# Kernel tuning notes

Measured on AMD Instinct MI355X. Metric: run time of the kernel, lower is better.

The kernel has to match this reference:

```python
import jax, jax.numpy as jnp
import numpy as np

N = 40000   # nodes
E = 640000  # edges (before self-loops)
G = 64      # graphs
EPS = 1e-5


def _gat_conv(x, src, dst, W, a_src, a_dst, bias, n_nodes):
    """PyG GATConv, heads=1, leaky_relu slope 0.2, with self-loops already in src/dst."""
    h = x @ W.T                              # [N, out]
    s_score = h @ a_src                      # [N]
    d_score = h @ a_dst                      # [N]
    e = jax.nn.leaky_relu(s_score[src] + d_score[dst], 0.2)  # [E]
    m = jax.ops.segment_max(e, dst, num_segments=n_nodes)
    ex = jnp.exp(e - m[dst])
    z = jax.ops.segment_sum(ex, dst, num_segments=n_nodes)
    alpha = ex / z[dst]                      # per-dst softmax over incoming edges
    out = jax.ops.segment_sum(h[src] * alpha[:, None], dst, num_segments=n_nodes)
    return out + bias


def _layer_norm(x, gamma, beta):
    mu = jnp.mean(x, axis=-1, keepdims=True)
    var = jnp.mean((x - mu) ** 2, axis=-1, keepdims=True)
    return gamma * (x - mu) * jax.lax.rsqrt(var + EPS) + beta


def setup_inputs() -> dict:
    key = jax.random.key(0)
    ks = jax.random.split(key, 16)
    x = jax.random.normal(ks[0], (N, 128), dtype=jnp.float32)
    edge_index = jax.random.randint(ks[1], (2, E), 0, N, dtype=jnp.int32)
    batch = jnp.sort(jax.random.randint(ks[2], (N,), 0, G, dtype=jnp.int32))
    def glorot(k, shape):
        fan = shape[-1]
        return jax.random.normal(k, shape, dtype=jnp.float32) / jnp.sqrt(jnp.float32(fan))
    return {
        "x": x, "edge_index": edge_index, "batch": batch,
        "W1": glorot(ks[3], (128, 128)), "a1_src": glorot(ks[4], (128,)),
        "a1_dst": glorot(ks[5], (128,)), "b1": jnp.zeros((128,), jnp.float32),
        "g1": jnp.ones((128,), jnp.float32), "be1": jnp.zeros((128,), jnp.float32),
        "W2": glorot(ks[6], (64, 128)), "a2_src": glorot(ks[7], (64,)),
        "a2_dst": glorot(ks[8], (64,)), "b2": jnp.zeros((64,), jnp.float32),
        "g2": jnp.ones((64,), jnp.float32), "be2": jnp.zeros((64,), jnp.float32),
        "Wl": glorot(ks[9], (64, 64)), "bl": jnp.zeros((64,), jnp.float32),
        "Wc": glorot(ks[10], (1, 64)), "bc": jnp.zeros((1,), jnp.float32),
    }


def reference(x, edge_index, batch, W1, a1_src, a1_dst, b1, g1, be1,
              W2, a2_src, a2_dst, b2, g2, be2, Wl, bl, Wc, bc):
    # add self-loops as PyG GATConv does by default
    loops = jnp.arange(N, dtype=edge_index.dtype)
    src = jnp.concatenate([edge_index[0], loops])
    dst = jnp.concatenate([edge_index[1], loops])

    h = jax.nn.relu(_gat_conv(x, src, dst, W1, a1_src, a1_dst, b1, N))
    h = _layer_norm(h, g1, be1)
    h = jax.nn.relu(_gat_conv(h, src, dst, W2, a2_src, a2_dst, b2, N))
    h = _layer_norm(h, g2, be2)

    # global mean pool over graphs
    sums = jax.ops.segment_sum(h, batch, num_segments=G)          # [G, 64]
    cnt = jax.ops.segment_sum(jnp.ones((N,), h.dtype), batch, num_segments=G)
    pooled = sums / jnp.maximum(cnt, 1.0)[:, None]

    out = pooled @ Wl.T + bl
    out = out @ Wc.T + bc                                          # [G, 1]
    return out.squeeze(-1)                                         # [G]
```

## Files before the change

kernel.cpp:

```cpp
#include <hip/hip_runtime.h>
#include <hip/hip_fp16.h>
#include <math.h>

#define NNODES 40000
#define NEDGES 640000
#define NGRAPH 64
#define CAP 96
constexpr float LN_EPS = 1e-5f;


typedef _Float16 v8h __attribute__((ext_vector_type(8)));
typedef float    v4f __attribute__((ext_vector_type(4)));

__device__ __forceinline__ float bf_sum(float v) {
    #pragma unroll
    for (int o = 32; o > 0; o >>= 1) v += __shfl_xor(v, o);
    return v;
}

__global__ void prep(const float* __restrict__ W1, const float* __restrict__ W2,
                     _Float16* __restrict__ Bf1, _Float16* __restrict__ Bf2,
                     int* __restrict__ cnt, float* __restrict__ sums) {
    int t = blockIdx.x * 256 + threadIdx.x;
    if (t < NNODES) cnt[t] = 0;
    if (t < 128 * 128) {
        const int o = t >> 7, k = t & 127;
        const int nt = o >> 4, lc = o & 15;
        const int ks = k >> 5, g = (k >> 3) & 3, j = k & 7;
        Bf1[(size_t)(((nt * 4 + ks) * 64 + g * 16 + lc) * 8 + j)] = (_Float16)W1[t];
    }
    if (t < 64 * 128) {
        const int o = t >> 7, k = t & 127;
        const int nt = o >> 4, lc = o & 15;
        const int ks = k >> 5, g = (k >> 3) & 3, j = k & 7;
        Bf2[(size_t)(((nt * 4 + ks) * 64 + g * 16 + lc) * 8 + j)] = (_Float16)W2[t];
    }
    if (t < NGRAPH * 64) sums[t] = 0.f;
}

__global__ void bin_edges(const int* __restrict__ ei, int E,
                          int* __restrict__ cnt, unsigned short* __restrict__ ssrc) {
    int e = blockIdx.x * blockDim.x + threadIdx.x;
    if (e >= E) return;
    int s = ei[e], d = ei[E + e];
    int pos = atomicAdd(cnt + d, 1);
    if (pos < CAP) ssrc[d * CAP + pos] = (unsigned short)s;
}

template<int DOUT>
__global__ __launch_bounds__(256) void gemm_scores_mfma(
        const float* __restrict__ X, const _Float16* __restrict__ Bfrag,
        const float* __restrict__ asrc, const float* __restrict__ adst,
        __half* __restrict__ H, float* __restrict__ S, float* __restrict__ Dv) {
    constexpr int NT = DOUT / 16;
    const int lane = threadIdx.x & 63;
    const int wv   = threadIdx.x >> 6;
    const int nb   = blockIdx.x * 64 + wv * 16;
    const int lc = lane & 15, g = lane >> 4;

    v8h a[4];
    const float* xr = X + (size_t)(nb + lc) * 128 + g * 8;
    #pragma unroll
    for (int ks = 0; ks < 4; ++ks) {
        const float4 lo = *(const float4*)(xr + ks * 32);
        const float4 hi = *(const float4*)(xr + ks * 32 + 4);
        v8h av;
        av[0] = (_Float16)lo.x; av[1] = (_Float16)lo.y;
        av[2] = (_Float16)lo.z; av[3] = (_Float16)lo.w;
        av[4] = (_Float16)hi.x; av[5] = (_Float16)hi.y;
        av[6] = (_Float16)hi.z; av[7] = (_Float16)hi.w;
        a[ks] = av;
    }

    v4f acc[NT];
    #pragma unroll
    for (int nt = 0; nt < NT; ++nt) acc[nt] = (v4f){0.f, 0.f, 0.f, 0.f};

    #pragma unroll
    for (int ks = 0; ks < 4; ++ks) {
        #pragma unroll
        for (int nt = 0; nt < NT; ++nt) {
            const v8h bv = *(const v8h*)(Bfrag + (size_t)(((nt * 4 + ks) * 64 + lane) * 8));
            acc[nt] = __builtin_amdgcn_mfma_f32_16x16x32_f16(a[ks], bv, acc[nt], 0, 0, 0);
        }
    }

    float sp[4] = {0.f, 0.f, 0.f, 0.f}, dp[4] = {0.f, 0.f, 0.f, 0.f};
    #pragma unroll
    for (int nt = 0; nt < NT; ++nt) {
        const float as_ = asrc[nt * 16 + lc];
        const float ad_ = adst[nt * 16 + lc];
        #pragma unroll
        for (int r = 0; r < 4; ++r) {
            const float hv = acc[nt][r];
            H[(size_t)(nb + g * 4 + r) * DOUT + nt * 16 + lc] = __float2half_rn(hv);
            sp[r] += hv * as_;
            dp[r] += hv * ad_;
        }
    }
    #pragma unroll
    for (int o = 8; o > 0; o >>= 1) {
        #pragma unroll
        for (int r = 0; r < 4; ++r) {
            sp[r] += __shfl_xor(sp[r], o);
            dp[r] += __shfl_xor(dp[r], o);
        }
    }
    #pragma unroll
    for (int r = 0; r < 4; ++r) {
        if (lc == r) {
            S[nb + g * 4 + r]  = sp[r];
            Dv[nb + g * 4 + r] = dp[r];
        }
    }
}

template<int D>
__device__ __forceinline__ void aggr_one_generic(
        const int node, const int deg, const int lane,
        const unsigned short* __restrict__ ssrc, const float* __restrict__ S,
        const float dsc, const __half* __restrict__ H,
        float& acc0, float& acc1, float& z) {
    constexpr int VPL = D / 64;
    float zz = 0.f;
    const int r0 = node * CAP;
    for (int bse = 0; bse < deg; bse += 64) {
        const int n = min(64, deg - bse);
        int s = 0; float a = 0.f;
        if (lane < n) {
            s = ssrc[r0 + bse + lane];
            float t = S[s] + dsc;
            t = t > 0.f ? t : 0.2f * t;
            a = __expf(t);
        }
        zz += bf_sum(a);
        const int abits = __float_as_int(a);
        for (int j = 0; j < n; ++j) {
            const int sj = __builtin_amdgcn_readlane(s, j);
            const float aj = __int_as_float(__builtin_amdgcn_readlane(abits, j));
            const __half* hp = H + (size_t)sj * D;
            if (VPL == 1) {
                acc0 += aj * __half2float(hp[lane]);
            } else {
                const float2 f = __half22float2(*(const __half2*)(hp + 2 * lane));
                acc0 += aj * f.x; acc1 += aj * f.y;
            }
        }
    }
    z = zz;
}

template<int D, int POOL>
__device__ __forceinline__ void finish_node(
        const int node, const int lane,
        float acc0, float acc1, float z, const float aself, const float2 selfF,
        const float* __restrict__ b, const float* __restrict__ gam,
        const float* __restrict__ bet,
        float* __restrict__ out, const int* __restrict__ batch,
        float* __restrict__ sums) {
    constexpr int VPL = D / 64;
    acc0 += aself * selfF.x;
    if (VPL == 2) acc1 += aself * selfF.y;
    z += aself;
    const float zinv = 1.0f / z;
    float vv[VPL], lsum = 0.f;
    vv[0] = acc0;
    if (VPL == 2) vv[1] = acc1;
    #pragma unroll
    for (int k = 0; k < VPL; ++k) {
        const int ch = VPL * lane + k;
        vv[k] = fmaxf(vv[k] * zinv + b[ch], 0.f);
        lsum += vv[k];
    }
    const float mu = bf_sum(lsum) / D;
    float q = 0.f;
    #pragma unroll
    for (int k = 0; k < VPL; ++k) { vv[k] -= mu; q += vv[k] * vv[k]; }
    const float rstd = rsqrtf(bf_sum(q) / D + LN_EPS);
    #pragma unroll
    for (int k = 0; k < VPL; ++k) {
        const int ch = VPL * lane + k;
        vv[k] = gam[ch] * vv[k] * rstd + bet[ch];
    }
    if (POOL) {
        const int bg = batch[node];
        atomicAdd(&sums[bg * D + lane], vv[0]);
    } else {
        if (VPL == 1) out[(size_t)node * D + lane] = vv[0];
        else *(float2*)(out + (size_t)node * D + 2 * lane) = make_float2(vv[0], vv[1]);
    }
}

template<int D, int POOL>
__global__ __launch_bounds__(256) void gat_aggr(
        const int* __restrict__ cnt, const unsigned short* __restrict__ ssrc,
        const float* __restrict__ S, const float* __restrict__ Dv,
        const __half* __restrict__ H,
        const float* __restrict__ b, const float* __restrict__ gam,
        const float* __restrict__ bet,
        float* __restrict__ out, const int* __restrict__ batch,
        float* __restrict__ sums) {
    constexpr int VPL = D / 64;
    const int lane = threadIdx.x & 63;
    const int wv   = threadIdx.x >> 6;
    const int nodeA = blockIdx.x * 8 + wv * 2;
    const int nodeB = nodeA + 1;

    const int degA = min(__builtin_amdgcn_readfirstlane(cnt[nodeA]), CAP);
    const int degB = min(__builtin_amdgcn_readfirstlane(cnt[nodeB]), CAP);
    const float dscA = Dv[nodeA], dscB = Dv[nodeB];

    float tsA = S[nodeA] + dscA; tsA = tsA > 0.f ? tsA : 0.2f * tsA;
    float tsB = S[nodeB] + dscB; tsB = tsB > 0.f ? tsB : 0.2f * tsB;
    const float aselfA = __expf(tsA);
    const float aselfB = __expf(tsB);

    float2 selfFA, selfFB;
    if (VPL == 1) {
        selfFA = make_float2(__half2float(H[(size_t)nodeA * D + lane]), 0.f);
        selfFB = make_float2(__half2float(H[(size_t)nodeB * D + lane]), 0.f);
    } else {
        selfFA = __half22float2(*(const __half2*)(H + (size_t)nodeA * D + 2 * lane));
        selfFB = __half22float2(*(const __half2*)(H + (size_t)nodeB * D + 2 * lane));
    }

    float accA0 = 0.f, accA1 = 0.f, accB0 = 0.f, accB1 = 0.f;
    float zA, zB;

    if (degA <= 64 && degB <= 64) {
        int sA = 0, sB = 0;
        if (lane < degA) sA = ssrc[nodeA * CAP + lane];
        if (lane < degB) sB = ssrc[nodeB * CAP + lane];
        float tA = S[sA] + dscA;
        float tB = S[sB] + dscB;
        tA = tA > 0.f ? tA : 0.2f * tA;
        tB = tB > 0.f ? tB : 0.2f * tB;
        const float aA = (lane < degA) ? __expf(tA) : 0.f;
        const float aB = (lane < degB) ? __expf(tB) : 0.f;
        zA = bf_sum(aA);
        zB = bf_sum(aB);
        const int abA = __float_as_int(aA), abB = __float_as_int(aB);

        const int nmA = (degA + 7) & ~7;
        const int nmB = (degB + 7) & ~7;
        const int nmax = max(nmA, nmB);
        for (int j = 0; j < nmax; j += 8) {
            const bool doA = j < nmA, doB = j < nmB;
            float afA[8], afB[8];
            __half2 hvA[8], hvB[8];
            __half hsA[8], hsB[8];
            if (doA) {
                #pragma unroll
                for (int u = 0; u < 8; ++u) {
                    const int sj = __builtin_amdgcn_readlane(sA, j + u);
                    afA[u] = __int_as_float(__builtin_amdgcn_readlane(abA, j + u));
                    const __half* hp = H + (size_t)sj * D;
                    if (VPL == 1) hsA[u] = hp[lane];
                    else          hvA[u] = *(const __half2*)(hp + 2 * lane);
                }
            }
            if (doB) {
                #pragma unroll
                for (int u = 0; u < 8; ++u) {
                    const int sj = __builtin_amdgcn_readlane(sB, j + u);
                    afB[u] = __int_as_float(__builtin_amdgcn_readlane(abB, j + u));
                    const __half* hp = H + (size_t)sj * D;
                    if (VPL == 1) hsB[u] = hp[lane];
                    else          hvB[u] = *(const __half2*)(hp + 2 * lane);
                }
            }
            if (doA) {
                #pragma unroll
                for (int u = 0; u < 8; ++u) {
                    if (VPL == 1) {
                        accA0 += afA[u] * __half2float(hsA[u]);
                    } else {
                        accA0 += afA[u] * __half2float(__low2half(hvA[u]));
                        accA1 += afA[u] * __half2float(__high2half(hvA[u]));
                    }
                }
            }
            if (doB) {
                #pragma unroll
                for (int u = 0; u < 8; ++u) {
                    if (VPL == 1) {
                        accB0 += afB[u] * __half2float(hsB[u]);
                    } else {
                        accB0 += afB[u] * __half2float(__low2half(hvB[u]));
                        accB1 += afB[u] * __half2float(__high2half(hvB[u]));
                    }
                }
            }
        }
    } else {
        aggr_one_generic<D>(nodeA, degA, lane, ssrc, S, dscA, H, accA0, accA1, zA);
        aggr_one_generic<D>(nodeB, degB, lane, ssrc, S, dscB, H, accB0, accB1, zB);
    }

    finish_node<D, POOL>(nodeA, lane, accA0, accA1, zA, aselfA, selfFA,
                         b, gam, bet, out, batch, sums);
    finish_node<D, POOL>(nodeB, lane, accB0, accB1, zB, aselfB, selfFB,
                         b, gam, bet, out, batch, sums);
}

__global__ void final_head(const float* __restrict__ sums, const int* __restrict__ batch,
                           const float* __restrict__ Wl, const float* __restrict__ bl,
                           const float* __restrict__ Wc, const float* __restrict__ bc,
                           float* __restrict__ out) {
    __shared__ float p[64];
    __shared__ float red[64];
    const int g = blockIdx.x, tid = threadIdx.x;
    int lo = 0, hi = NNODES;
    while (lo < hi) { int mid = (lo + hi) >> 1; if (batch[mid] < g) lo = mid + 1; else hi = mid; }
    int lo2 = lo, hi2 = NNODES;
    while (lo2 < hi2) { int mid = (lo2 + hi2) >> 1; if (batch[mid] < g + 1) lo2 = mid + 1; else hi2 = mid; }
    const float cnt = (float)(lo2 - lo);
    p[tid] = sums[g * 64 + tid] / fmaxf(cnt, 1.0f);
    __syncthreads();
    float t = bl[tid];
    #pragma unroll 8
    for (int k = 0; k < 64; ++k) t += Wl[tid * 64 + k] * p[k];
    red[tid] = Wc[tid] * t;
    __syncthreads();
    for (int s = 32; s > 0; s >>= 1) {
        if (tid < s) red[tid] += red[tid + s];
        __syncthreads();
    }
    if (tid == 0) out[g] = red[0] + bc[0];
}

extern "C" void kernel_launch(void* const* d_in, const int* in_sizes, int n_in,
                              void* d_out, int out_size, void* d_ws, size_t ws_size,
                              hipStream_t stream) {
    const int N = NNODES, E = NEDGES, G = NGRAPH;

    const float* x      = (const float*)d_in[0];
    const int*   ei     = (const int*)d_in[1];
    const int*   batch  = (const int*)d_in[2];
    const float* W1     = (const float*)d_in[3];
    const float* a1s    = (const float*)d_in[4];
    const float* a1d    = (const float*)d_in[5];
    const float* b1     = (const float*)d_in[6];
    const float* g1     = (const float*)d_in[7];
    const float* be1    = (const float*)d_in[8];
    const float* W2     = (const float*)d_in[9];
    const float* a2s    = (const float*)d_in[10];
    const float* a2d    = (const float*)d_in[11];
    const float* b2     = (const float*)d_in[12];
    const float* g2     = (const float*)d_in[13];
    const float* be2    = (const float*)d_in[14];
    const float* Wl     = (const float*)d_in[15];
    const float* bl     = (const float*)d_in[16];
    const float* Wc     = (const float*)d_in[17];
    const float* bc     = (const float*)d_in[18];

    char* w = (char*)d_ws;
    __half* h1  = (__half*)w; w += (size_t)N * 128 * 2;
    float* acc1 = (float*)w; w += (size_t)N * 128 * 4;
    float* S    = (float*)w; w += (size_t)N * 4;
    float* Dv   = (float*)w; w += (size_t)N * 4;
    int* cnt    = (int*)w;   w += (size_t)N * 4;
    unsigned short* ssrc = (unsigned short*)w; w += (size_t)N * CAP * 2;
    _Float16* Bf1 = (_Float16*)w; w += (size_t)128 * 128 * 2;
    _Float16* Bf2 = (_Float16*)w; w += (size_t)64 * 128 * 2;
    float* sums = (float*)w; w += (size_t)G * 64 * 4;
    __half* h2 = h1;

    const int TB = 256;
    const int gridN = (N + 255) / 256;

    prep<<<gridN, 256, 0, stream>>>(W1, W2, Bf1, Bf2, cnt, sums);

    bin_edges<<<(E + TB - 1) / TB, TB, 0, stream>>>(ei, E, cnt, ssrc);

    gemm_scores_mfma<128><<<N / 64, 256, 0, stream>>>(x, Bf1, a1s, a1d, h1, S, Dv);
    gat_aggr<128, 0><<<N / 8, 256, 0, stream>>>(cnt, ssrc, S, Dv, h1, b1, g1, be1,
                                                acc1, nullptr, nullptr);

    gemm_scores_mfma<64><<<N / 64, 256, 0, stream>>>(acc1, Bf2, a2s, a2d, h2, S, Dv);
    gat_aggr<64, 1><<<N / 8, 256, 0, stream>>>(cnt, ssrc, S, Dv, h2, b2, g2, be2,
                                               nullptr, batch, sums);

    final_head<<<G, 64, 0, stream>>>(sums, batch, Wl, bl, Wc, bc, (float*)d_out);
}
```

Baseline: 245.6 us.

## Fuse layer-2 projection and scores into layer-1 aggregation; merge prep with binning

Layer-1 aggregation now applies bias, ReLU and LayerNorm, then does the 128->64 W2 projection and the attention scores in-kernel from an fp16 W2 copy in LDS. This removes the fp32 acc1 round trip and the second MFMA GEMM launch. Prep and edge binning become one kernel plus a memset, and the gather loop handles two nodes per wave with 8-way unrolled loads. In exchange, every block reconverts W2 into LDS and runs a scalar 64x64 dot loop per node, which adds LDS traffic and work per block.

```diff
diff --git a/kernel.cpp b/kernel.cpp
--- a/kernel.cpp
+++ b/kernel.cpp
@@ -18,33 +18,23 @@
     return v;
 }
 
-__global__ void prep(const float* __restrict__ W1, const float* __restrict__ W2,
-                     _Float16* __restrict__ Bf1, _Float16* __restrict__ Bf2,
-                     int* __restrict__ cnt, float* __restrict__ sums) {
-    int t = blockIdx.x * 256 + threadIdx.x;
-    if (t < NNODES) cnt[t] = 0;
+__global__ void bin_prep(const int* __restrict__ ei, int E,
+                         int* __restrict__ cnt, unsigned short* __restrict__ ssrc,
+                         const float* __restrict__ W1, _Float16* __restrict__ Bf1,
+                         float* __restrict__ sums) {
+    const int t = blockIdx.x * blockDim.x + threadIdx.x;
     if (t < 128 * 128) {
         const int o = t >> 7, k = t & 127;
         const int nt = o >> 4, lc = o & 15;
         const int ks = k >> 5, g = (k >> 3) & 3, j = k & 7;
         Bf1[(size_t)(((nt * 4 + ks) * 64 + g * 16 + lc) * 8 + j)] = (_Float16)W1[t];
     }
-    if (t < 64 * 128) {
-        const int o = t >> 7, k = t & 127;
-        const int nt = o >> 4, lc = o & 15;
-        const int ks = k >> 5, g = (k >> 3) & 3, j = k & 7;
-        Bf2[(size_t)(((nt * 4 + ks) * 64 + g * 16 + lc) * 8 + j)] = (_Float16)W2[t];
-    }
     if (t < NGRAPH * 64) sums[t] = 0.f;
-}
-
-__global__ void bin_edges(const int* __restrict__ ei, int E,
-                          int* __restrict__ cnt, unsigned short* __restrict__ ssrc) {
-    int e = blockIdx.x * blockDim.x + threadIdx.x;
-    if (e >= E) return;
-    int s = ei[e], d = ei[E + e];
-    int pos = atomicAdd(cnt + d, 1);
-    if (pos < CAP) ssrc[d * CAP + pos] = (unsigned short)s;
+    if (t < E) {
+        const int s = ei[t], d = ei[E + t];
+        const int pos = atomicAdd(cnt + d, 1);
+        if (pos < CAP) ssrc[d * CAP + pos] = (unsigned short)s;
+    }
 }
 
 template<int DOUT>
@@ -148,6 +138,144 @@
         }
     }
     z = zz;
+}
+
+__device__ __forceinline__ void finish_fuse(
+        const int node, const int lane, const int wv,
+        float acc0, float acc1, float z, const float aself, const float2 selfF,
+        const float* __restrict__ b, const float* __restrict__ gam,
+        const float* __restrict__ bet,
+        const float* __restrict__ a2s, const float* __restrict__ a2d,
+        const __half2 (*W2h)[65], float2 (*vwf)[64],
+        __half* __restrict__ H2, float* __restrict__ S2, float* __restrict__ Dv2) {
+    acc0 += aself * selfF.x;
+    acc1 += aself * selfF.y;
+    z += aself;
+    const float zinv = 1.0f / z;
+    float v0 = fmaxf(acc0 * zinv + b[2 * lane],     0.f);
+    float v1 = fmaxf(acc1 * zinv + b[2 * lane + 1], 0.f);
+    const float mu = bf_sum(v0 + v1) * (1.f / 128.f);
+    v0 -= mu; v1 -= mu;
+    const float rstd = rsqrtf(bf_sum(v0 * v0 + v1 * v1) * (1.f / 128.f) + LN_EPS);
+    v0 = gam[2 * lane]     * v0 * rstd + bet[2 * lane];
+    v1 = gam[2 * lane + 1] * v1 * rstd + bet[2 * lane + 1];
+
+    vwf[wv][lane] = make_float2(v0, v1);
+    asm volatile("s_waitcnt lgkmcnt(0)" ::: "memory");
+    float h2 = 0.f;
+    #pragma unroll
+    for (int c2 = 0; c2 < 64; ++c2) {
+        const float2 vp = vwf[wv][c2];
+        const float2 wf = __half22float2(W2h[lane][c2]);
+        h2 += vp.x * wf.x + vp.y * wf.y;
+    }
+    H2[(size_t)node * 64 + lane] = __float2half_rn(h2);
+    const float s2 = bf_sum(h2 * a2s[lane]);
+    const float d2 = bf_sum(h2 * a2d[lane]);
+    if (lane == 0) { S2[node] = s2; Dv2[node] = d2; }
+}
+
+__global__ __launch_bounds__(256) void gat_aggr_fuse(
+        const int* __restrict__ cnt, const unsigned short* __restrict__ ssrc,
+        const float* __restrict__ S, const float* __restrict__ Dv,
+        const __half* __restrict__ H,
+        const float* __restrict__ b, const float* __restrict__ gam,
+        const float* __restrict__ bet,
+        const float* __restrict__ W2,
+        const float* __restrict__ a2s, const float* __restrict__ a2d,
+        __half* __restrict__ H2, float* __restrict__ S2, float* __restrict__ Dv2) {
+    constexpr int D = 128;
+    __shared__ __half2 W2h[64][65];
+    __shared__ float2 vwf[4][64];
+
+    for (int i = threadIdx.x; i < 64 * 64; i += 256) {
+        const int o = i >> 6, c2 = i & 63;
+        const float2 wf = *(const float2*)(W2 + o * 128 + 2 * c2);
+        W2h[o][c2] = __floats2half2_rn(wf.x, wf.y);
+    }
+    __syncthreads();
+
+    const int lane = threadIdx.x & 63;
+    const int wv   = threadIdx.x >> 6;
+    const int nodeA = blockIdx.x * 8 + wv * 2;
+    const int nodeB = nodeA + 1;
+
+    const int degA = min(__builtin_amdgcn_readfirstlane(cnt[nodeA]), CAP);
+    const int degB = min(__builtin_amdgcn_readfirstlane(cnt[nodeB]), CAP);
+    const float dscA = Dv[nodeA], dscB = Dv[nodeB];
+
+    float tsA = S[nodeA] + dscA; tsA = tsA > 0.f ? tsA : 0.2f * tsA;
+    float tsB = S[nodeB] + dscB; tsB = tsB > 0.f ? tsB : 0.2f * tsB;
+    const float aselfA = __expf(tsA);
+    const float aselfB = __expf(tsB);
+
+    const float2 selfFA = __half22float2(*(const __half2*)(H + (size_t)nodeA * D + 2 * lane));
+    const float2 selfFB = __half22float2(*(const __half2*)(H + (size_t)nodeB * D + 2 * lane));
+
+    float accA0 = 0.f, accA1 = 0.f, accB0 = 0.f, accB1 = 0.f;
+    float zA, zB;
+
+    if (degA <= 64 && degB <= 64) {
+        int sA = 0, sB = 0;
+        if (lane < degA) sA = ssrc[nodeA * CAP + lane];
+        if (lane < degB) sB = ssrc[nodeB * CAP + lane];
+        float tA = S[sA] + dscA;
+        float tB = S[sB] + dscB;
+        tA = tA > 0.f ? tA : 0.2f * tA;
+        tB = tB > 0.f ? tB : 0.2f * tB;
+        const float aA = (lane < degA) ? __expf(tA) : 0.f;
+        const float aB = (lane < degB) ? __expf(tB) : 0.f;
+        zA = bf_sum(aA);
+        zB = bf_sum(aB);
+        const int abA = __float_as_int(aA), abB = __float_as_int(aB);
+
+        const int nmA = (degA + 7) & ~7;
+        const int nmB = (degB + 7) & ~7;
+        const int nmax = max(nmA, nmB);
+        for (int j = 0; j < nmax; j += 8) {
+            const bool doA = j < nmA, doB = j < nmB;
+            float afA[8], afB[8];
+            __half2 hvA[8], hvB[8];
+            if (doA) {
+                #pragma unroll
+                for (int u = 0; u < 8; ++u) {
+                    const int sj = __builtin_amdgcn_readlane(sA, j + u);
+                    afA[u] = __int_as_float(__builtin_amdgcn_readlane(abA, j + u));
+                    hvA[u] = *(const __half2*)(H + (size_t)sj * D + 2 * lane);
+                }
+            }
+            if (doB) {
+                #pragma unroll
+                for (int u = 0; u < 8; ++u) {
+                    const int sj = __builtin_amdgcn_readlane(sB, j + u);
+                    afB[u] = __int_as_float(__builtin_amdgcn_readlane(abB, j + u));
+                    hvB[u] = *(const __half2*)(H + (size_t)sj * D + 2 * lane);
+                }
+            }
+            if (doA) {
+                #pragma unroll
+                for (int u = 0; u < 8; ++u) {
+                    const float2 f = __half22float2(hvA[u]);
+                    accA0 += afA[u] * f.x; accA1 += afA[u] * f.y;
+                }
+            }
+            if (doB) {
+                #pragma unroll
+                for (int u = 0; u < 8; ++u) {
+                    const float2 f = __half22float2(hvB[u]);
+                    accB0 += afB[u] * f.x; accB1 += afB[u] * f.y;
+                }
+            }
+        }
+    } else {
+        aggr_one_generic<D>(nodeA, degA, lane, ssrc, S, dscA, H, accA0, accA1, zA);
+        aggr_one_generic<D>(nodeB, degB, lane, ssrc, S, dscB, H, accB0, accB1, zB);
+    }
+
+    finish_fuse(nodeA, lane, wv, accA0, accA1, zA, aselfA, selfFA,
+                b, gam, bet, a2s, a2d, W2h, vwf, H2, S2, Dv2);
+    finish_fuse(nodeB, lane, wv, accB0, accB1, zB, aselfB, selfFB,
+                b, gam, bet, a2s, a2d, W2h, vwf, H2, S2, Dv2);
 }
 
 template<int D, int POOL>
@@ -356,29 +484,27 @@
 
     char* w = (char*)d_ws;
     __half* h1  = (__half*)w; w += (size_t)N * 128 * 2;
-    float* acc1 = (float*)w; w += (size_t)N * 128 * 4;
-    float* S    = (float*)w; w += (size_t)N * 4;
-    float* Dv   = (float*)w; w += (size_t)N * 4;
+    __half* h2  = (__half*)w; w += (size_t)N * 64 * 2;
+    float* S1   = (float*)w; w += (size_t)N * 4;
+    float* Dv1  = (float*)w; w += (size_t)N * 4;
+    float* S2   = (float*)w; w += (size_t)N * 4;
+    float* Dv2  = (float*)w; w += (size_t)N * 4;
     int* cnt    = (int*)w;   w += (size_t)N * 4;
     unsigned short* ssrc = (unsigned short*)w; w += (size_t)N * CAP * 2;
     _Float16* Bf1 = (_Float16*)w; w += (size_t)128 * 128 * 2;
-    _Float16* Bf2 = (_Float16*)w; w += (size_t)64 * 128 * 2;
     float* sums = (float*)w; w += (size_t)G * 64 * 4;
-    __half* h2 = h1;
 
     const int TB = 256;
-    const int gridN = (N + 255) / 256;
-
-    prep<<<gridN, 256, 0, stream>>>(W1, W2, Bf1, Bf2, cnt, sums);
-
-    bin_edges<<<(E + TB - 1) / TB, TB, 0, stream>>>(ei, E, cnt, ssrc);
-
-    gemm_scores_mfma<128><<<N / 64, 256, 0, stream>>>(x, Bf1, a1s, a1d, h1, S, Dv);
-    gat_aggr<128, 0><<<N / 8, 256, 0, stream>>>(cnt, ssrc, S, Dv, h1, b1, g1, be1,
-                                                acc1, nullptr, nullptr);
-
-    gemm_scores_mfma<64><<<N / 64, 256, 0, stream>>>(acc1, Bf2, a2s, a2d, h2, S, Dv);
-    gat_aggr<64, 1><<<N / 8, 256, 0, stream>>>(cnt, ssrc, S, Dv, h2, b2, g2, be2,
+
+    hipMemsetAsync(cnt, 0, (size_t)N * 4, stream);
+    bin_prep<<<(E + TB - 1) / TB, TB, 0, stream>>>(ei, E, cnt, ssrc, W1, Bf1, sums);
+
+    gemm_scores_mfma<128><<<N / 64, 256, 0, stream>>>(x, Bf1, a1s, a1d, h1, S1, Dv1);
+
+    gat_aggr_fuse<<<N / 8, 256, 0, stream>>>(cnt, ssrc, S1, Dv1, h1, b1, g1, be1,
+                                             W2, a2s, a2d, h2, S2, Dv2);
+
+    gat_aggr<64, 1><<<N / 8, 256, 0, stream>>>(cnt, ssrc, S2, Dv2, h2, b2, g2, be2,
                                                nullptr, batch, sums);
 
     final_head<<<G, 64, 0, stream>>>(sums, batch, Wl, bl, Wc, bc, (float*)d_out);
```

After: 257.2 us. 1.05x slower.

## Store layer-1 output in fp16, stage GEMM input via LDS, fuse prep with binning

Applied to the files above, without the earlier changes.

The layer-1 aggregation now writes its normalized output as fp16 instead of fp32, which halves that intermediate's write and its re-read by the second GEMM. The GEMM kernel stages the input tile through shared memory with coalesced row loads instead of strided per-lane float loads. The prep and edge-binning kernels are merged into one launch, with the count array cleared by a memset. This adds an fp16 rounding step on the layer-1 activations, a block barrier and shared-memory use in the GEMM, and separate buffers for each layer's scores.

```diff
diff --git a/kernel.cpp b/kernel.cpp
--- a/kernel.cpp
+++ b/kernel.cpp
@@ -18,11 +18,12 @@
     return v;
 }
 
-__global__ void prep(const float* __restrict__ W1, const float* __restrict__ W2,
-                     _Float16* __restrict__ Bf1, _Float16* __restrict__ Bf2,
-                     int* __restrict__ cnt, float* __restrict__ sums) {
-    int t = blockIdx.x * 256 + threadIdx.x;
-    if (t < NNODES) cnt[t] = 0;
+__global__ void bin_prep(const int* __restrict__ ei, int E,
+                         int* __restrict__ cnt, unsigned short* __restrict__ ssrc,
+                         const float* __restrict__ W1, const float* __restrict__ W2,
+                         _Float16* __restrict__ Bf1, _Float16* __restrict__ Bf2,
+                         float* __restrict__ sums) {
+    const int t = blockIdx.x * blockDim.x + threadIdx.x;
     if (t < 128 * 128) {
         const int o = t >> 7, k = t & 127;
         const int nt = o >> 4, lc = o & 15;
@@ -36,41 +37,50 @@
         Bf2[(size_t)(((nt * 4 + ks) * 64 + g * 16 + lc) * 8 + j)] = (_Float16)W2[t];
     }
     if (t < NGRAPH * 64) sums[t] = 0.f;
-}
-
-__global__ void bin_edges(const int* __restrict__ ei, int E,
-                          int* __restrict__ cnt, unsigned short* __restrict__ ssrc) {
-    int e = blockIdx.x * blockDim.x + threadIdx.x;
-    if (e >= E) return;
-    int s = ei[e], d = ei[E + e];
-    int pos = atomicAdd(cnt + d, 1);
-    if (pos < CAP) ssrc[d * CAP + pos] = (unsigned short)s;
-}
-
-template<int DOUT>
+    if (t < E) {
+        const int s = ei[t], d = ei[E + t];
+        const int pos = atomicAdd(cnt + d, 1);
+        if (pos < CAP) ssrc[d * CAP + pos] = (unsigned short)s;
+    }
+}
+
+template<int DOUT, bool F16IN>
 __global__ __launch_bounds__(256) void gemm_scores_mfma(
-        const float* __restrict__ X, const _Float16* __restrict__ Bfrag,
+        const void* __restrict__ Xin, const _Float16* __restrict__ Bfrag,
         const float* __restrict__ asrc, const float* __restrict__ adst,
         __half* __restrict__ H, float* __restrict__ S, float* __restrict__ Dv) {
     constexpr int NT = DOUT / 16;
-    const int lane = threadIdx.x & 63;
-    const int wv   = threadIdx.x >> 6;
-    const int nb   = blockIdx.x * 64 + wv * 16;
+    __shared__ _Float16 xs[64][136];
+    const int tid = threadIdx.x;
+    const int base = blockIdx.x * 64;
+
+    if (F16IN) {
+        const _Float16* Xh = (const _Float16*)Xin;
+        for (int c = tid; c < 64 * 16; c += 256) {
+            const int row = c >> 4, c8 = c & 15;
+            *(float4*)&xs[row][c8 * 8] =
+                *(const float4*)(Xh + (size_t)(base + row) * 128 + c8 * 8);
+        }
+    } else {
+        const float* Xf = (const float*)Xin;
+        for (int c = tid; c < 64 * 32; c += 256) {
+            const int row = c >> 5, c4 = c & 31;
+            const float4 v = *(const float4*)(Xf + (size_t)(base + row) * 128 + c4 * 4);
+            _Float16 h4[4] = {(_Float16)v.x, (_Float16)v.y, (_Float16)v.z, (_Float16)v.w};
+            *(uint2*)&xs[row][c4 * 4] = *(const uint2*)h4;
+        }
+    }
+    __syncthreads();
+
+    const int lane = tid & 63;
+    const int wv   = tid >> 6;
+    const int nb   = base + wv * 16;
     const int lc = lane & 15, g = lane >> 4;
 
     v8h a[4];
-    const float* xr = X + (size_t)(nb + lc) * 128 + g * 8;
-    #pragma unroll
-    for (int ks = 0; ks < 4; ++ks) {
-        const float4 lo = *(const float4*)(xr + ks * 32);
-        const float4 hi = *(const float4*)(xr + ks * 32 + 4);
-        v8h av;
-        av[0] = (_Float16)lo.x; av[1] = (_Float16)lo.y;
-        av[2] = (_Float16)lo.z; av[3] = (_Float16)lo.w;
-        av[4] = (_Float16)hi.x; av[5] = (_Float16)hi.y;
-        av[6] = (_Float16)hi.z; av[7] = (_Float16)hi.w;
-        a[ks] = av;
-    }
+    #pragma unroll
+    for (int ks = 0; ks < 4; ++ks)
+        a[ks] = *(const v8h*)&xs[wv * 16 + lc][ks * 32 + g * 8];
 
     v4f acc[NT];
     #pragma unroll
@@ -156,7 +166,7 @@
         float acc0, float acc1, float z, const float aself, const float2 selfF,
         const float* __restrict__ b, const float* __restrict__ gam,
         const float* __restrict__ bet,
-        float* __restrict__ out, const int* __restrict__ batch,
+        __half* __restrict__ outh, const int* __restrict__ batch,
         float* __restrict__ sums) {
     constexpr int VPL = D / 64;
     acc0 += aself * selfF.x;
@@ -186,8 +196,11 @@
         const int bg = batch[node];
         atomicAdd(&sums[bg * D + lane], vv[0]);
     } else {
-        if (VPL == 1) out[(size_t)node * D + lane] = vv[0];
-        else *(float2*)(out + (size_t)node * D + 2 * lane) = make_float2(vv[0], vv[1]);
+        if (VPL == 2)
+            *(__half2*)(outh + (size_t)node * D + 2 * lane) =
+                __floats2half2_rn(vv[0], vv[1]);
+        else
+            outh[(size_t)node * D + lane] = __float2half_rn(vv[0]);
     }
 }
 
@@ -198,7 +211,7 @@
         const __half* __restrict__ H,
         const float* __restrict__ b, const float* __restrict__ gam,
         const float* __restrict__ bet,
-        float* __restrict__ out, const int* __restrict__ batch,
+        __half* __restrict__ outh, const int* __restrict__ batch,
         float* __restrict__ sums) {
     constexpr int VPL = D / 64;
     const int lane = threadIdx.x & 63;
@@ -298,9 +311,9 @@
     }
 
     finish_node<D, POOL>(nodeA, lane, accA0, accA1, zA, aselfA, selfFA,
-                         b, gam, bet, out, batch, sums);
+                         b, gam, bet, outh, batch, sums);
     finish_node<D, POOL>(nodeB, lane, accB0, accB1, zB, aselfB, selfFB,
-                         b, gam, bet, out, batch, sums);
+                         b, gam, bet, outh, batch, sums);
 }
 
 __global__ void final_head(const float* __restrict__ sums, const int* __restrict__ batch,
@@ -355,30 +368,35 @@
     const float* bc     = (const float*)d_in[18];
 
     char* w = (char*)d_ws;
-    __half* h1  = (__half*)w; w += (size_t)N * 128 * 2;
-    float* acc1 = (float*)w; w += (size_t)N * 128 * 4;
-    float* S    = (float*)w; w += (size_t)N * 4;
-    float* Dv   = (float*)w; w += (size_t)N * 4;
-    int* cnt    = (int*)w;   w += (size_t)N * 4;
+    __half* h1   = (__half*)w; w += (size_t)N * 128 * 2;
+    __half* v1h  = (__half*)w; w += (size_t)N * 128 * 2;
+    __half* h2   = (__half*)w; w += (size_t)N * 64 * 2;
+    float* S1    = (float*)w; w += (size_t)N * 4;
+    float* Dv1   = (float*)w; w += (size_t)N * 4;
+    float* S2    = (float*)w; w += (size_t)N * 4;
+    float* Dv2   = (float*)w; w += (size_t)N * 4;
+    int* cnt     = (int*)w;   w += (size_t)N * 4;
     unsigned short* ssrc = (unsigned short*)w; w += (size_t)N * CAP * 2;
     _Float16* Bf1 = (_Float16*)w; w += (size_t)128 * 128 * 2;
     _Float16* Bf2 = (_Float16*)w; w += (size_t)64 * 128 * 2;
-    float* sums = (float*)w; w += (size_t)G * 64 * 4;
-    __half* h2 = h1;
+    float* sums  = (float*)w; w += (size_t)G * 64 * 4;
 
     const int TB = 256;
-    const int gridN = (N + 255) / 256;
-
-    prep<<<gridN, 256, 0, stream>>>(W1, W2, Bf1, Bf2, cnt, sums);
-
-    bin_edges<<<(E + TB - 1) / TB, TB, 0, stream>>>(ei, E, cnt, ssrc);
-
-    gemm_scores_mfma<128><<<N / 64, 256, 0, stream>>>(x, Bf1, a1s, a1d, h1, S, Dv);
-    gat_aggr<128, 0><<<N / 8, 256, 0, stream>>>(cnt, ssrc, S, Dv, h1, b1, g1, be1,
-                                                acc1, nullptr, nullptr);
-
-    gemm_scores_mfma<64><<<N / 64, 256, 0, stream>>>(acc1, Bf2, a2s, a2d, h2, S, Dv);
-    gat_aggr<64, 1><<<N / 8, 256, 0, stream>>>(cnt, ssrc, S, Dv, h2, b2, g2, be2,
+
+    hipMemsetAsync(cnt, 0, (size_t)N * 4, stream);
+    bin_prep<<<(E + TB - 1) / TB, TB, 0, stream>>>(ei, E, cnt, ssrc, W1, W2,
+                                                   Bf1, Bf2, sums);
+
+    gemm_scores_mfma<128, false><<<N / 64, 256, 0, stream>>>(x, Bf1, a1s, a1d,
+                                                             h1, S1, Dv1);
+
+    gat_aggr<128, 0><<<N / 8, 256, 0, stream>>>(cnt, ssrc, S1, Dv1, h1, b1, g1, be1,
+                                                v1h, nullptr, nullptr);
+
+    gemm_scores_mfma<64, true><<<N / 64, 256, 0, stream>>>(v1h, Bf2, a2s, a2d,
+                                                           h2, S2, Dv2);
+
+    gat_aggr<64, 1><<<N / 8, 256, 0, stream>>>(cnt, ssrc, S2, Dv2, h2, b2, g2, be2,
                                                nullptr, batch, sums);
 
     final_head<<<G, 64, 0, stream>>>(sums, batch, Wl, bl, Wc, bc, (float*)d_out);
```

Result: no change. 243.8 us (median of 2 runs) (-0.7%).
